# Kernel optimization log

Measured on AMD Instinct MI355X. Metric: run time of the kernel, lower is better.

The kernel has to match this reference:

```python
import jax, jax.numpy as jnp
import numpy as np

N, E, NF, EF, G = 50000, 400000, 128, 64, 200


def _leaky(x):
    return jax.nn.leaky_relu(x, 0.01)


def _edge_softmax(logits, dst, n):
    # softmax over edges grouped by destination node; logits: [E, 1]
    m = jax.ops.segment_max(logits, dst, num_segments=n)
    m = jnp.where(jnp.isfinite(m), m, 0.0)  # guard empty segments
    e = jnp.exp(logits - m[dst])
    s = jax.ops.segment_sum(e, dst, num_segments=n)
    return e / s[dst]


def _gru(x, h, Wx, Wh, bx, bh):
    # torch.nn.GRUCell gate order: (r, z, n)
    gx = x @ Wx + bx
    gh = h @ Wh + bh
    H = h.shape[-1]
    r = jax.nn.sigmoid(gx[:, :H] + gh[:, :H])
    z = jax.nn.sigmoid(gx[:, H:2 * H] + gh[:, H:2 * H])
    nn_ = jnp.tanh(gx[:, 2 * H:] + r * gh[:, 2 * H:])
    return (1.0 - z) * nn_ + z * h


def setup_inputs() -> dict:
    key = jax.random.key(0)
    ks = jax.random.split(key, 20)
    f32 = jnp.float32
    w = lambda k, s: (jax.random.normal(k, s) * 0.05).astype(f32)
    z = lambda s: jnp.zeros(s, f32)
    return {
        "node_feats": jax.random.normal(ks[0], (N, NF), f32),
        "edge_feats": jax.random.normal(ks[1], (E, EF), f32),
        "gc_node_W": w(ks[4], (NF, G)), "gc_node_b": z((G,)),
        "gc_e1_W": w(ks[5], (NF + EF, G)), "gc_e1_b": z((G,)),
        "gc_e2_W": w(ks[6], (2 * G, 1)), "gc_e2_b": z((1,)),
        "gc_et_W": w(ks[7], (G, G)), "gc_et_b": z((G,)),
        "gc_gru_Wx": w(ks[8], (G, 3 * G)), "gc_gru_Wh": w(ks[9], (G, 3 * G)),
        "gc_gru_bx": z((3 * G,)), "gc_gru_bh": z((3 * G,)),
        "l1_e_W": w(ks[10], (2 * G, 1)), "l1_e_b": z((1,)),
        "l1_pn_W": w(ks[11], (G, G)), "l1_pn_b": z((G,)),
        "l1_gru_Wx": w(ks[12], (G, 3 * G)), "l1_gru_Wh": w(ks[13], (G, 3 * G)),
        "l1_gru_bx": z((3 * G,)), "l1_gru_bh": z((3 * G,)),
        "l1_bn_g": jnp.ones((G,), f32), "l1_bn_b": z((G,)),
        "src": jax.random.randint(ks[2], (E,), 0, N, jnp.int32),
        "dst": jax.random.randint(ks[3], (E,), 0, N, jnp.int32),
    }


def reference(node_feats, edge_feats,
              gc_node_W, gc_node_b, gc_e1_W, gc_e1_b, gc_e2_W, gc_e2_b,
              gc_et_W, gc_et_b, gc_gru_Wx, gc_gru_Wh, gc_gru_bx, gc_gru_bh,
              l1_e_W, l1_e_b, l1_pn_W, l1_pn_b, l1_gru_Wx, l1_gru_Wh,
              l1_gru_bx, l1_gru_bh, l1_bn_g, l1_bn_b, src, dst):
    n = node_feats.shape[0]
    # ---- GetContext ----
    hv_new = _leaky(node_feats @ gc_node_W + gc_node_b)                      # [N, G]
    he1 = _leaky(jnp.concatenate([node_feats[src], edge_feats], 1)
                 @ gc_e1_W + gc_e1_b)                                        # [E, G]
    logits = _leaky(jnp.concatenate([hv_new[dst], he1], 1)
                    @ gc_e2_W + gc_e2_b)                                     # [E, 1]
    a = _edge_softmax(logits, dst, n)
    e = a * (he1 @ gc_et_W + gc_et_b)
    c = jax.ops.segment_sum(e, dst, num_segments=n)                          # [N, G]
    h0 = jax.nn.relu(_gru(jax.nn.elu(c), hv_new,
                          gc_gru_Wx, gc_gru_Wh, gc_gru_bx, gc_gru_bh))
    # ---- GNNLayer ----
    logits2 = _leaky(jnp.concatenate([h0[dst], h0[src]], 1) @ l1_e_W + l1_e_b)
    a2 = _edge_softmax(logits2, dst, n) + 1.0
    hvp = h0 @ l1_pn_W + l1_pn_b
    c2 = jax.ops.segment_sum(hvp[src] * a2, dst, num_segments=n)
    h1 = jax.nn.relu(_gru(jax.nn.elu(c2), h0,
                          l1_gru_Wx, l1_gru_Wh, l1_gru_bx, l1_gru_bh))
    # BatchNorm1d (training-mode batch stats, eps=1e-5)
    mu = h1.mean(0)
    var = h1.var(0)
    h1 = l1_bn_g * (h1 - mu) / jnp.sqrt(var + 1e-5) + l1_bn_b
    return h0 + h1
```

## Files before the change

kernel.cpp:

```cpp
#include <hip/hip_runtime.h>
#include <math.h>

#define G 200
#define NF 128
#define EF 64

typedef __attribute__((ext_vector_type(8))) short bf16x8;
typedef __attribute__((ext_vector_type(4))) float f32x4;

__device__ __forceinline__ float leakyf(float x) { return x > 0.f ? x : 0.01f * x; }
__device__ __forceinline__ float eluf(float x)   { return x > 0.f ? x : (expf(x) - 1.f); }
__device__ __forceinline__ float sigm(float x)   { return 1.f / (1.f + expf(-x)); }

__device__ __forceinline__ unsigned short f2bf(float x) {
    union { float f; unsigned int u; } v; v.f = x;
    unsigned int r = v.u + 0x7FFF + ((v.u >> 16) & 1);
    return (unsigned short)(r >> 16);
}
__device__ __forceinline__ float bf2f(unsigned short u) {
    union { unsigned int i; float f; } v; v.i = ((unsigned int)u) << 16;
    return v.f;
}
__device__ __forceinline__ unsigned int pk2(float a, float b) {
    return (unsigned int)f2bf(a) | ((unsigned int)f2bf(b) << 16);
}

__global__ __launch_bounds__(256) void tprep_k(
    const float* __restrict__ W, unsigned short* __restrict__ Wt,
    int Kreal, int kpad, int Nstride, int Nreal)
{
    int total = 208 * kpad;
    for (int i = blockIdx.x * 256 + threadIdx.x; i < total; i += gridDim.x * 256) {
        int n = i / kpad, k = i % kpad;
        Wt[i] = (n < Nreal && k < Kreal) ? f2bf(W[(size_t)k * Nstride + n]) : 0;
    }
}

__global__ __launch_bounds__(256) void wgru3_k(
    const float* __restrict__ Wx, const float* __restrict__ Wh,
    unsigned short* __restrict__ Btrz, unsigned short* __restrict__ Btn)
{
    const int total = 512 * 416;
    for (int i = blockIdx.x * 256 + threadIdx.x; i < total; i += gridDim.x * 256) {
        int n = i / 416, k = i % 416;
        float v = 0.f;
        if (n < 416) {
            int gg = (n >= 208) ? 1 : 0;
            int c = n - gg * 208;
            if (c < 200) {
                if (k < 200)                  v = Wx[(size_t)k * 600 + gg * 200 + c];
                else if (k >= 208 && k < 408) v = Wh[(size_t)(k - 208) * 600 + gg * 200 + c];
            }
        }
        Btrz[i] = f2bf(v);

        float u = 0.f;
        int s = n >> 4, cc = n & 15;
        if (s < 26) {
            int c = (s >> 1) * 16 + cc;
            if (c < 200) {
                if (!(s & 1)) { if (k < 200) u = Wx[(size_t)k * 600 + 400 + c]; }
                else { if (k >= 208 && k < 408) u = Wh[(size_t)(k - 208) * 600 + 400 + c]; }
            }
        }
        Btn[i] = f2bf(u);
    }
}

__global__ __launch_bounds__(256) void gpack_k(
    const float* __restrict__ X, const float* __restrict__ H,
    unsigned short* __restrict__ Apk, int M, int Mpad)
{
    const long total = (long)Mpad * 52;
    for (long i = (long)blockIdx.x * 256 + threadIdx.x; i < total;
         i += (long)gridDim.x * 256) {
        int row = (int)(i / 52), ch = (int)(i % 52);
        uint4 u = make_uint4(0, 0, 0, 0);
        if (row < M) {
            if (ch < 25) {
                const float4* xp = (const float4*)(X + (size_t)row * 200 + ch * 8);
                float4 a = xp[0], b = xp[1];
                u.x = pk2(eluf(a.x), eluf(a.y)); u.y = pk2(eluf(a.z), eluf(a.w));
                u.z = pk2(eluf(b.x), eluf(b.y)); u.w = pk2(eluf(b.z), eluf(b.w));
            } else if (ch >= 26 && ch < 51) {
                const float4* hp = (const float4*)(H + (size_t)row * 200 + (ch - 26) * 8);
                float4 a = hp[0], b = hp[1];
                u.x = pk2(a.x, a.y); u.y = pk2(a.z, a.w);
                u.z = pk2(b.x, b.y); u.w = pk2(b.z, b.w);
            }
        }
        *(uint4*)&Apk[(size_t)row * 416 + ch * 8] = u;
    }
}

template <int EPI>
__global__ __launch_bounds__(256) void tgemm_k(
    const unsigned short* __restrict__ Apk,
    const unsigned short* __restrict__ Bt,
    const float* __restrict__ bx, const float* __restrict__ bh,
    unsigned short* __restrict__ RZ,
    float* __restrict__ OUT, int M)
{
    __shared__ __align__(16) unsigned short As[2][128 * 32];
    __shared__ __align__(16) unsigned short Bs[2][128 * 32];

    const int tid = threadIdx.x;
    const int w = tid >> 6, lane = tid & 63, l15 = lane & 15, lq = lane >> 4;
    const int wr = w >> 1, wc = w & 1;
    const int bm = blockIdx.x * 128, bn = blockIdx.y * 128;
    const int r0 = tid >> 2, sl = tid & 3;

    f32x4 acc[4][4];
#pragma unroll
    for (int a = 0; a < 4; ++a)
#pragma unroll
        for (int b = 0; b < 4; ++b) acc[a][b] = (f32x4){0.f, 0.f, 0.f, 0.f};

    {
        uint4 pa0 = *(const uint4*)&Apk[(size_t)(bm + r0) * 416 + sl * 8];
        uint4 pa1 = *(const uint4*)&Apk[(size_t)(bm + 64 + r0) * 416 + sl * 8];
        uint4 pb0 = *(const uint4*)&Bt[(size_t)(bn + r0) * 416 + sl * 8];
        uint4 pb1 = *(const uint4*)&Bt[(size_t)(bn + 64 + r0) * 416 + sl * 8];
        int w0 = sl ^ ((r0 >> 1) & 3), w1 = sl ^ (((r0 + 64) >> 1) & 3);
        *(uint4*)&As[0][r0 * 32 + w0 * 8] = pa0;
        *(uint4*)&As[0][(r0 + 64) * 32 + w1 * 8] = pa1;
        *(uint4*)&Bs[0][r0 * 32 + w0 * 8] = pb0;
        *(uint4*)&Bs[0][(r0 + 64) * 32 + w1 * 8] = pb1;
    }
    __syncthreads();

    int cur = 0;
    for (int c = 0; c < 13; ++c) {
        uint4 pa0, pa1, pb0, pb1;
        if (c < 12) {
            int kc = (c + 1) * 32;
            pa0 = *(const uint4*)&Apk[(size_t)(bm + r0) * 416 + kc + sl * 8];
            pa1 = *(const uint4*)&Apk[(size_t)(bm + 64 + r0) * 416 + kc + sl * 8];
            pb0 = *(const uint4*)&Bt[(size_t)(bn + r0) * 416 + kc + sl * 8];
            pb1 = *(const uint4*)&Bt[(size_t)(bn + 64 + r0) * 416 + kc + sl * 8];
        }
        bf16x8 af[4], bfr[4];
#pragma unroll
        for (int s = 0; s < 4; ++s) {
            int ra = wr * 64 + s * 16 + l15;
            af[s] = *(const bf16x8*)&As[cur][ra * 32 + (lq ^ ((ra >> 1) & 3)) * 8];
            int rb = wc * 64 + s * 16 + l15;
            bfr[s] = *(const bf16x8*)&Bs[cur][rb * 32 + (lq ^ ((rb >> 1) & 3)) * 8];
        }
#pragma unroll
        for (int sr = 0; sr < 4; ++sr)
#pragma unroll
            for (int sc = 0; sc < 4; ++sc)
                acc[sr][sc] = __builtin_amdgcn_mfma_f32_16x16x32_bf16(
                    af[sr], bfr[sc], acc[sr][sc], 0, 0, 0);

        if (c < 12) {
            int nb = cur ^ 1;
            int w0 = sl ^ ((r0 >> 1) & 3), w1 = sl ^ (((r0 + 64) >> 1) & 3);
            *(uint4*)&As[nb][r0 * 32 + w0 * 8] = pa0;
            *(uint4*)&As[nb][(r0 + 64) * 32 + w1 * 8] = pa1;
            *(uint4*)&Bs[nb][r0 * 32 + w0 * 8] = pb0;
            *(uint4*)&Bs[nb][(r0 + 64) * 32 + w1 * 8] = pb1;
        }
        __syncthreads();
        cur ^= 1;
    }

    if (EPI == 0) {
#pragma unroll
        for (int sr = 0; sr < 4; ++sr)
#pragma unroll
            for (int sc = 0; sc < 4; ++sc) {
                int col = bn + wc * 64 + sc * 16 + l15;
                if (col >= 416) continue;
                float bsum = (col < 208) ? (bx[col] + bh[col])
                                         : (bx[col - 8] + bh[col - 8]);
#pragma unroll
                for (int i = 0; i < 4; ++i) {
                    int row = bm + wr * 64 + sr * 16 + lq * 4 + i;
                    if (row < M)
                        RZ[(size_t)row * 416 + col] = f2bf(sigm(acc[sr][sc][i] + bsum));
                }
            }
    } else {
#pragma unroll
        for (int p = 0; p < 2; ++p) {
            int sglob = (bn >> 4) + wc * 4 + 2 * p;
            int cc = (sglob >> 1) * 16 + l15;
            if (cc >= 200) continue;
            float bxn = bx[400 + cc], bhn = bh[400 + cc];
#pragma unroll
            for (int sr = 0; sr < 4; ++sr)
#pragma unroll
                for (int i = 0; i < 4; ++i) {
                    int row = bm + wr * 64 + sr * 16 + lq * 4 + i;
                    if (row >= M) continue;
                    float rr = bf2f(RZ[(size_t)row * 416 + cc]);
                    float zz = bf2f(RZ[(size_t)row * 416 + 208 + cc]);
                    float hh = bf2f(Apk[(size_t)row * 416 + 208 + cc]);
                    float nn = tanhf(acc[sr][2 * p][i] + bxn +
                                     rr * (acc[sr][2 * p + 1][i] + bhn));
                    float o = (1.f - zz) * nn + zz * hh;
                    OUT[(size_t)row * 200 + cc] = fmaxf(o, 0.f);
                }
        }
    }
}

__global__ __launch_bounds__(256) void hist_k(
    const int* __restrict__ dst, int* __restrict__ cnt, int E)
{
    int i = blockIdx.x * 256 + threadIdx.x;
    if (i < E) atomicAdd(&cnt[dst[i]], 1);
}

__global__ __launch_bounds__(256) void scan_k(
    const int* __restrict__ cnt, int* __restrict__ offs,
    int* __restrict__ cursor, int Nn)
{
    __shared__ int wsum[4];
    const int tid = threadIdx.x;
    const int lane = tid & 63, wv = tid >> 6;
    int carry = 0;
    const int CH = 8;
    for (int base = 0; base < Nn; base += 256 * CH) {
        int v[CH]; int tsum = 0;
        int i0 = base + tid * CH;
#pragma unroll
        for (int j = 0; j < CH; ++j) {
            v[j] = (i0 + j < Nn) ? cnt[i0 + j] : 0;
            tsum += v[j];
        }
        int x = tsum;
        for (int off = 1; off < 64; off <<= 1) {
            int t = __shfl_up(x, off);
            if (lane >= off) x += t;
        }
        if (lane == 63) wsum[wv] = x;
        __syncthreads();
        int wbase = 0;
#pragma unroll
        for (int wq = 0; wq < 4; ++wq) wbase += (wq < wv) ? wsum[wq] : 0;
        int gtot = wsum[0] + wsum[1] + wsum[2] + wsum[3];
        int run = carry + wbase + (x - tsum);
#pragma unroll
        for (int j = 0; j < CH; ++j) {
            int idx = i0 + j;
            if (idx < Nn) { offs[idx] = run; cursor[idx] = run; }
            run += v[j];
        }
        carry += gtot;
        __syncthreads();
    }
    if (tid == 0) offs[Nn] = carry;
}

__global__ __launch_bounds__(256) void scatter_k(
    const int* __restrict__ src, const int* __restrict__ dst,
    int* __restrict__ cursor, int* __restrict__ eidC,
    int* __restrict__ srcC, int* __restrict__ dstC, int E)
{
    int i = blockIdx.x * 256 + threadIdx.x;
    if (i < E) {
        int d = dst[i];
        int pos = atomicAdd(&cursor[d], 1);
        eidC[pos] = i; srcC[pos] = src[i]; dstC[pos] = d;
    }
}

__global__ __launch_bounds__(256) void mgemm_k(
    const float* __restrict__ X, const unsigned short* __restrict__ Wt,
    const float* __restrict__ bias, float* __restrict__ OUT,
    int M, int Kreal, int kch, int astr, int leaky,
    const float* __restrict__ xdiv)
{
    __shared__ __align__(16) unsigned short A[64 * 232];
    const int tid = threadIdx.x;
    const int w = tid >> 6, lane = tid & 63, l15 = lane & 15, lq = lane >> 4;
    const int bm = blockIdx.x * 64;
    const int kpad = kch * 32;
    const int nch8 = Kreal >> 3;

    for (int i = tid; i < 64 * nch8; i += 256) {
        int r = i / nch8, ch = i % nch8;
        int grow = bm + r;
        uint4 u = make_uint4(0, 0, 0, 0);
        if (grow < M) {
            const float4* xp = (const float4*)(X + (size_t)grow * Kreal + ch * 8);
            float inv = 1.f;
            if (xdiv) { float dv = xdiv[grow]; inv = (dv > 0.f) ? 1.f / dv : 0.f; }
            float4 a = xp[0], b = xp[1];
            u.x = pk2(a.x * inv, a.y * inv); u.y = pk2(a.z * inv, a.w * inv);
            u.z = pk2(b.x * inv, b.y * inv); u.w = pk2(b.z * inv, b.w * inv);
        }
        *(uint4*)&A[r * astr + ch * 8] = u;
    }
    if (tid < 64) {
        for (int p = Kreal; p < kpad; p += 8)
            *(uint4*)&A[tid * astr + p] = make_uint4(0, 0, 0, 0);
    }
    __syncthreads();

    const int arow = (w * 16 + l15) * astr;
    f32x4 acc[13];
#pragma unroll
    for (int t = 0; t < 13; ++t) acc[t] = (f32x4){0.f, 0.f, 0.f, 0.f};

    for (int c = 0; c < kch; ++c) {
        bf16x8 a = *(const bf16x8*)&A[arow + c * 32 + lq * 8];
#pragma unroll
        for (int t = 0; t < 13; ++t) {
            bf16x8 b = *(const bf16x8*)&Wt[(size_t)(t * 16 + l15) * kpad + c * 32 + lq * 8];
            acc[t] = __builtin_amdgcn_mfma_f32_16x16x32_bf16(a, b, acc[t], 0, 0, 0);
        }
    }

    float rg[4];
#pragma unroll
    for (int i = 0; i < 4; ++i) {
        int grow = bm + w * 16 + lq * 4 + i;
        rg[i] = 1.f;
        if (xdiv && grow < M) rg[i] = (xdiv[grow] > 0.f) ? 1.f : 0.f;
    }

#pragma unroll
    for (int t = 0; t < 13; ++t) {
        int col = t * 16 + l15;
        if (col >= 200) continue;
        float bs = bias[col];
#pragma unroll
        for (int i = 0; i < 4; ++i) {
            int grow = bm + w * 16 + lq * 4 + i;
            if (grow >= M) continue;
            float v = acc[t][i] + bs * rg[i];
            OUT[(size_t)grow * 200 + col] = leaky ? leakyf(v) : v;
        }
    }
}

__global__ __launch_bounds__(256) void hd_k(
    const float* __restrict__ x, const float* __restrict__ W,
    float* __restrict__ hd, int Nn)
{
    int wid = blockIdx.x * 4 + (threadIdx.x >> 6);
    int lane = threadIdx.x & 63;
    if (wid >= Nn) return;
    float s = 0.f;
    for (int j = lane; j < G; j += 64) s += x[(size_t)wid * G + j] * W[j];
    for (int off = 32; off; off >>= 1) s += __shfl_down(s, off);
    if (lane == 0) hd[wid] = s;
}

__global__ __launch_bounds__(256) void edgefuse2_k(
    const float* __restrict__ node, const float* __restrict__ edgef,
    const int* __restrict__ srcC, const int* __restrict__ dstC,
    const int* __restrict__ eidC,
    const unsigned short* __restrict__ W1t, const float* __restrict__ b1,
    const float* __restrict__ e2W, const float* __restrict__ e2b,
    const float* __restrict__ hd,
    float* __restrict__ sden, float* __restrict__ hacc, int E)
{
    __shared__ __align__(16) unsigned short U[64 * 216];
    __shared__ __align__(16) unsigned short Wt[208 * 40];
    __shared__ float rowlg[64];
    __shared__ float pexp_s[64];
    __shared__ int   dst_s[64];

    const int tid  = threadIdx.x;
    const int w    = tid >> 6;
    const int lane = tid & 63;
    const int l15  = lane & 15;
    const int lq   = lane >> 4;
    const int eb   = blockIdx.x * 64;

    {
        const int r4 = tid >> 2, q = tid & 3;
        const int pos = eb + r4;
        if (pos < E) {
            const int se = srcC[pos];
            const int ei = eidC[pos];
            const float4* np = (const float4*)(node + (size_t)se * NF);
            const float4* ep = (const float4*)(edgef + (size_t)ei * EF);
            uint4* rowp = (uint4*)(U + r4 * 216);
#pragma unroll
            for (int i = 0; i < 4; ++i) {
                float4 a = np[q * 8 + 2 * i];
                float4 b = np[q * 8 + 2 * i + 1];
                uint4 u; u.x = pk2(a.x, a.y); u.y = pk2(a.z, a.w);
                u.z = pk2(b.x, b.y); u.w = pk2(b.z, b.w);
                rowp[q * 4 + i] = u;
            }
            uint4* edp = (uint4*)(U + r4 * 216 + 128);
#pragma unroll
            for (int i = 0; i < 2; ++i) {
                float4 a = ep[q * 4 + 2 * i];
                float4 b = ep[q * 4 + 2 * i + 1];
                uint4 u; u.x = pk2(a.x, a.y); u.y = pk2(a.z, a.w);
                u.z = pk2(b.x, b.y); u.w = pk2(b.z, b.w);
                edp[q * 2 + i] = u;
            }
        } else {
            uint4 z = make_uint4(0, 0, 0, 0);
            uint4* rowp = (uint4*)(U + r4 * 216);
#pragma unroll
            for (int i = 0; i < 4; ++i) rowp[q * 4 + i] = z;
            uint4* edp = (uint4*)(U + r4 * 216 + 128);
            edp[q * 2] = z; edp[q * 2 + 1] = z;
        }
        if (tid < 64) dst_s[tid] = (eb + tid < E) ? dstC[eb + tid] : -1;
    }
    __syncthreads();

    f32x4 acc[13];
#pragma unroll
    for (int t = 0; t < 13; ++t) acc[t] = (f32x4){0.f, 0.f, 0.f, 0.f};

    for (int c = 0; c < 6; ++c) {
        for (int q = tid; q < 832; q += 256) {
            int n = q >> 2, s = q & 3;
            *(uint4*)(Wt + n * 40 + s * 8) =
                *(const uint4*)(W1t + (size_t)n * 192 + c * 32 + s * 8);
        }
        __syncthreads();
        bf16x8 a = *(const bf16x8*)(U + (w * 16 + l15) * 216 + c * 32 + lq * 8);
#pragma unroll
        for (int t = 0; t < 13; ++t) {
            bf16x8 b = *(const bf16x8*)(Wt + (t * 16 + l15) * 40 + lq * 8);
            acc[t] = __builtin_amdgcn_mfma_f32_16x16x32_bf16(a, b, acc[t], 0, 0, 0);
        }
        __syncthreads();
    }

    float p[4] = {0.f, 0.f, 0.f, 0.f};
#pragma unroll
    for (int t = 0; t < 13; ++t) {
        const int col = t * 16 + l15;
#pragma unroll
        for (int r = 0; r < 4; ++r) {
            const int row = w * 16 + lq * 4 + r;
            float v = 0.f;
            if (col < 200) {
                v = leakyf(acc[t][r] + b1[col]);
                p[r] = fmaf(v, e2W[200 + col], p[r]);
            }
            U[row * 216 + col] = f2bf(v);
        }
    }
#pragma unroll
    for (int r = 0; r < 4; ++r) {
        p[r] += __shfl_xor(p[r], 1);
        p[r] += __shfl_xor(p[r], 2);
        p[r] += __shfl_xor(p[r], 4);
        p[r] += __shfl_xor(p[r], 8);
    }
    if (l15 == 0) {
#pragma unroll
        for (int r = 0; r < 4; ++r) rowlg[w * 16 + lq * 4 + r] = p[r];
    }
    __syncthreads();

    if (tid < 64) {
        float pe = 0.f;
        if (eb + tid < E) {
            float l = leakyf(rowlg[tid] + hd[dst_s[tid]] + e2b[0]);
            pe = expf(l);
            atomicAdd(&sden[dst_s[tid]], pe);
        }
        pexp_s[tid] = pe;
    }
    __syncthreads();

    if (tid < 200) {
        const int c = tid;
        float s = 0.f;
        int cur = dst_s[0];
        for (int r = 0; r < 64; ++r) {
            int d = dst_s[r];
            if (d < 0) break;
            if (d != cur) {
                atomicAdd(&hacc[(size_t)cur * 200 + c], s);
                s = 0.f; cur = d;
            }
            s = fmaf(pexp_s[r], bf2f(U[r * 216 + c]), s);
        }
        atomicAdd(&hacc[(size_t)cur * 200 + c], s);
    }
}

__global__ __launch_bounds__(256) void layer2_k(
    const float* __restrict__ h0, const float* __restrict__ hvp,
    const float* __restrict__ hd2,
    const float* __restrict__ W, const float* __restrict__ b,
    const int* __restrict__ offs, const int* __restrict__ srcC,
    float* __restrict__ c2, int Nn)
{
    __shared__ float pes[4][64];
    const int wv = threadIdx.x >> 6;
    const int lane = threadIdx.x & 63;
    const int n = blockIdx.x * 4 + wv;
    if (n >= Nn) return;

    const int base = offs[n], end = offs[n + 1];
    const float hdn = hd2[n] + b[0];

    float ssum = 0.f;
    for (int pos = base; pos < end; ++pos) {
        const float* hr = h0 + (size_t)srcC[pos] * 200;
        float part = hr[lane] * W[200 + lane]
                   + hr[64 + lane] * W[264 + lane]
                   + hr[128 + lane] * W[328 + lane];
        if (lane < 8) part += hr[192 + lane] * W[392 + lane];
        for (int off = 32; off; off >>= 1) part += __shfl_xor(part, off);
        float pe = expf(leakyf(part + hdn));
        ssum += pe;
        int i = pos - base;
        if (i < 64 && lane == 0) pes[wv][i] = pe;
    }
    float inv = (end > base) ? 1.f / ssum : 0.f;

    float a0 = 0.f, a1 = 0.f, a2v = 0.f, a3 = 0.f;
    for (int pos = base; pos < end; ++pos) {
        int i = pos - base;
        float pe;
        if (i < 64) pe = pes[wv][i];
        else {
            const float* hr = h0 + (size_t)srcC[pos] * 200;
            float part = hr[lane] * W[200 + lane]
                       + hr[64 + lane] * W[264 + lane]
                       + hr[128 + lane] * W[328 + lane];
            if (lane < 8) part += hr[192 + lane] * W[392 + lane];
            for (int off = 32; off; off >>= 1) part += __shfl_xor(part, off);
            pe = expf(leakyf(part + hdn));
        }
        float aw = pe * inv + 1.f;
        const float* vr = hvp + (size_t)srcC[pos] * 200;
        a0  += aw * vr[lane];
        a1  += aw * vr[64 + lane];
        a2v += aw * vr[128 + lane];
        if (lane < 8) a3 += aw * vr[192 + lane];
    }
    float* out = c2 + (size_t)n * 200;
    out[lane] = a0; out[64 + lane] = a1; out[128 + lane] = a2v;
    if (lane < 8) out[192 + lane] = a3;
}

__global__ __launch_bounds__(256) void bnstat_k(
    const float* __restrict__ h1, float* __restrict__ stats, long total)
{
    __shared__ float ls[2 * G];
    for (int t = threadIdx.x; t < 2 * G; t += 256) ls[t] = 0.f;
    __syncthreads();
    for (long idx = (long)blockIdx.x * 256 + threadIdx.x; idx < total;
         idx += (long)gridDim.x * 256) {
        float v = h1[idx];
        int c = (int)(idx % G);
        atomicAdd(&ls[c], v);
        atomicAdd(&ls[G + c], v * v);
    }
    __syncthreads();
    for (int t = threadIdx.x; t < 2 * G; t += 256) atomicAdd(&stats[t], ls[t]);
}

__global__ __launch_bounds__(256) void final_k(
    float* __restrict__ out, const float* __restrict__ h1,
    const float* __restrict__ stats,
    const float* __restrict__ g, const float* __restrict__ bb, int Nn)
{
    long total = (long)Nn * G;
    for (long idx = (long)blockIdx.x * 256 + threadIdx.x; idx < total;
         idx += (long)gridDim.x * 256) {
        int c = (int)(idx % G);
        float mu  = stats[c] / Nn;
        float var = stats[G + c] / Nn - mu * mu;
        float xh  = (h1[idx] - mu) * rsqrtf(var + 1e-5f);
        out[idx] = out[idx] + g[c] * xh + bb[c];
    }
}

extern "C" void kernel_launch(void* const* d_in, const int* in_sizes, int n_in,
                              void* d_out, int out_size, void* d_ws, size_t ws_size,
                              hipStream_t stream)
{
    const float* node_feats = (const float*)d_in[0];
    const float* edge_feats = (const float*)d_in[1];
    const float* gc_node_W  = (const float*)d_in[2];
    const float* gc_node_b  = (const float*)d_in[3];
    const float* gc_e1_W    = (const float*)d_in[4];
    const float* gc_e1_b    = (const float*)d_in[5];
    const float* gc_e2_W    = (const float*)d_in[6];
    const float* gc_e2_b    = (const float*)d_in[7];
    const float* gc_et_W    = (const float*)d_in[8];
    const float* gc_et_b    = (const float*)d_in[9];
    const float* gc_gru_Wx  = (const float*)d_in[10];
    const float* gc_gru_Wh  = (const float*)d_in[11];
    const float* gc_gru_bx  = (const float*)d_in[12];
    const float* gc_gru_bh  = (const float*)d_in[13];
    const float* l1_e_W     = (const float*)d_in[14];
    const float* l1_e_b     = (const float*)d_in[15];
    const float* l1_pn_W    = (const float*)d_in[16];
    const float* l1_pn_b    = (const float*)d_in[17];
    const float* l1_gru_Wx  = (const float*)d_in[18];
    const float* l1_gru_Wh  = (const float*)d_in[19];
    const float* l1_gru_bx  = (const float*)d_in[20];
    const float* l1_gru_bh  = (const float*)d_in[21];
    const float* l1_bn_g    = (const float*)d_in[22];
    const float* l1_bn_b    = (const float*)d_in[23];
    const int*   src        = (const int*)d_in[24];
    const int*   dst        = (const int*)d_in[25];

    const int Nn = in_sizes[0] / NF;
    const int E  = in_sizes[24];
    const int Mpad = ((Nn + 127) / 128) * 128;

    float* ws = (float*)d_ws;
    size_t o = 0;
    float* hv    = ws + o; o += (size_t)Nn * G;
    float* cbuf  = ws + o; o += ((size_t)Mpad * 416 + 1) / 2;
    unsigned short* rzbuf = (unsigned short*)cbuf;
    float* sden  = ws + o; o += (size_t)Nn;
    float* hd    = ws + o; o += (size_t)Nn;
    float* stats = ws + o; o += 512;
    unsigned short* W1t_g  = (unsigned short*)(ws + o); o += (208 * 192) / 2;
    unsigned short* etWt_g = (unsigned short*)(ws + o); o += (208 * 224) / 2;
    unsigned short* ncWt_g = (unsigned short*)(ws + o); o += (208 * 128) / 2;
    unsigned short* pnWt_g = (unsigned short*)(ws + o); o += (208 * 224) / 2;
    unsigned short* Btrz1  = (unsigned short*)(ws + o); o += (512 * 416) / 2;
    unsigned short* Btn1   = (unsigned short*)(ws + o); o += (512 * 416) / 2;
    unsigned short* Btrz2  = (unsigned short*)(ws + o); o += (512 * 416) / 2;
    unsigned short* Btn2   = (unsigned short*)(ws + o); o += (512 * 416) / 2;
    int* cnt    = (int*)(ws + o); o += (size_t)Nn;
    int* offs   = (int*)(ws + o); o += (size_t)Nn + 1;
    int* cursor = (int*)(ws + o); o += (size_t)Nn;
    int* eidC   = (int*)(ws + o); o += (size_t)E;
    int* srcC   = (int*)(ws + o); o += (size_t)E;
    int* dstC   = (int*)(ws + o); o += (size_t)E;
    unsigned short* apack = (unsigned short*)(ws + o); o += ((size_t)Mpad * 416 + 1) / 2;

    float* h0  = (float*)d_out;
    float* hvp = hv;
    float* h1  = hv;

    const int gN64 = (Nn + 63) / 64;
    const int gE64 = (E + 63) / 64;
    const int gE256 = (E + 255) / 256;
    const int nWaves = (Nn + 3) / 4;
    const long totNG = (long)Nn * G;
    const dim3 gGEMM((Mpad / 128), 4);

    hipMemsetAsync(cnt, 0, (size_t)Nn * sizeof(int), stream);
    tprep_k<<<128, 256, 0, stream>>>(gc_e1_W,   W1t_g,  192, 192, 200, 200);
    tprep_k<<<128, 256, 0, stream>>>(gc_et_W,   etWt_g, 200, 224, 200, 200);
    tprep_k<<<128, 256, 0, stream>>>(gc_node_W, ncWt_g, 128, 128, 200, 200);
    tprep_k<<<128, 256, 0, stream>>>(l1_pn_W,   pnWt_g, 200, 224, 200, 200);
    wgru3_k<<<256, 256, 0, stream>>>(gc_gru_Wx, gc_gru_Wh, Btrz1, Btn1);
    wgru3_k<<<256, 256, 0, stream>>>(l1_gru_Wx, l1_gru_Wh, Btrz2, Btn2);
    hist_k<<<gE256, 256, 0, stream>>>(dst, cnt, E);
    scan_k<<<1, 256, 0, stream>>>(cnt, offs, cursor, Nn);
    scatter_k<<<gE256, 256, 0, stream>>>(src, dst, cursor, eidC, srcC, dstC, E);

    hipMemsetAsync(sden, 0, (size_t)Nn * sizeof(float), stream);
    hipMemsetAsync(cbuf, 0, (size_t)Nn * G * sizeof(float), stream);
    hipMemsetAsync(stats, 0, 512 * sizeof(float), stream);

    mgemm_k<<<gN64, 256, 0, stream>>>(node_feats, ncWt_g, gc_node_b, hv,
                                      Nn, 128, 4, 136, 1, nullptr);
    hd_k<<<nWaves, 256, 0, stream>>>(hv, gc_e2_W, hd, Nn);

    edgefuse2_k<<<gE64, 256, 0, stream>>>(
        node_feats, edge_feats, srcC, dstC, eidC,
        W1t_g, gc_e1_b, gc_e2_W, gc_e2_b, hd, sden, cbuf, E);

    mgemm_k<<<gN64, 256, 0, stream>>>(cbuf, etWt_g, gc_et_b, cbuf,
                                      Nn, 200, 7, 232, 0, sden);

    gpack_k<<<2048, 256, 0, stream>>>(cbuf, hv, apack, Nn, Mpad);
    tgemm_k<0><<<gGEMM, 256, 0, stream>>>(apack, Btrz1, gc_gru_bx, gc_gru_bh,
                                          rzbuf, nullptr, Nn);
    tgemm_k<1><<<gGEMM, 256, 0, stream>>>(apack, Btn1, gc_gru_bx, gc_gru_bh,
                                          rzbuf, h0, Nn);

    hd_k<<<nWaves, 256, 0, stream>>>(h0, l1_e_W, hd, Nn);

    mgemm_k<<<gN64, 256, 0, stream>>>(h0, pnWt_g, l1_pn_b, hvp,
                                      Nn, 200, 7, 232, 0, nullptr);

    layer2_k<<<nWaves, 256, 0, stream>>>(h0, hvp, hd, l1_e_W, l1_e_b,
                                         offs, srcC, cbuf, Nn);

    gpack_k<<<2048, 256, 0, stream>>>(cbuf, h0, apack, Nn, Mpad);
    tgemm_k<0><<<gGEMM, 256, 0, stream>>>(apack, Btrz2, l1_gru_bx, l1_gru_bh,
                                          rzbuf, nullptr, Nn);
    tgemm_k<1><<<gGEMM, 256, 0, stream>>>(apack, Btn2, l1_gru_bx, l1_gru_bh,
                                          rzbuf, h1, Nn);

    bnstat_k<<<2048, 256, 0, stream>>>(h1, stats, totNG);
    final_k<<<2048, 256, 0, stream>>>((float*)d_out, h1, stats,
                                      l1_bn_g, l1_bn_b, Nn);
}
```

Before: 1.123 ms.

## Precompute per-node source logits, read weights directly, and simplify BN stats

Layer-2 attention logits are split algebraically into a per-destination term and a per-source scalar computed once per node. The edge loops now read one float per edge instead of a 200-wide row of h0 and skip the per-edge wave reductions. The edge-fused GEMM drops its LDS weight staging and barriers and loads B fragments straight from global memory, which relies on cache hits. Batch-norm statistics move from per-element shared-memory atomics to per-column register accumulation across rows.

Result: slower. 1.209 ms (+7.7%).

```diff
diff --git a/kernel.cpp b/kernel.cpp
--- a/kernel.cpp
+++ b/kernel.cpp
@@ -351,7 +351,7 @@
     if (lane == 0) hd[wid] = s;
 }
 
-__global__ __launch_bounds__(256) void edgefuse2_k(
+__global__ __launch_bounds__(256) void edgefuse3_k(
     const float* __restrict__ node, const float* __restrict__ edgef,
     const int* __restrict__ srcC, const int* __restrict__ dstC,
     const int* __restrict__ eidC,
@@ -361,7 +361,6 @@
     float* __restrict__ sden, float* __restrict__ hacc, int E)
 {
     __shared__ __align__(16) unsigned short U[64 * 216];
-    __shared__ __align__(16) unsigned short Wt[208 * 40];
     __shared__ float rowlg[64];
     __shared__ float pexp_s[64];
     __shared__ int   dst_s[64];
@@ -416,19 +415,12 @@
     for (int t = 0; t < 13; ++t) acc[t] = (f32x4){0.f, 0.f, 0.f, 0.f};
 
     for (int c = 0; c < 6; ++c) {
-        for (int q = tid; q < 832; q += 256) {
-            int n = q >> 2, s = q & 3;
-            *(uint4*)(Wt + n * 40 + s * 8) =
-                *(const uint4*)(W1t + (size_t)n * 192 + c * 32 + s * 8);
-        }
-        __syncthreads();
         bf16x8 a = *(const bf16x8*)(U + (w * 16 + l15) * 216 + c * 32 + lq * 8);
 #pragma unroll
         for (int t = 0; t < 13; ++t) {
-            bf16x8 b = *(const bf16x8*)(Wt + (t * 16 + l15) * 40 + lq * 8);
+            bf16x8 b = *(const bf16x8*)&W1t[(size_t)(t * 16 + l15) * 192 + c * 32 + lq * 8];
             acc[t] = __builtin_amdgcn_mfma_f32_16x16x32_bf16(a, b, acc[t], 0, 0, 0);
         }
-        __syncthreads();
     }
 
     float p[4] = {0.f, 0.f, 0.f, 0.f};
@@ -487,14 +479,13 @@
     }
 }
 
-__global__ __launch_bounds__(256) void layer2_k(
-    const float* __restrict__ h0, const float* __restrict__ hvp,
-    const float* __restrict__ hd2,
-    const float* __restrict__ W, const float* __restrict__ b,
+__global__ __launch_bounds__(256) void layer2b_k(
+    const float* __restrict__ hvp,
+    const float* __restrict__ hd2, const float* __restrict__ hs,
+    const float* __restrict__ b,
     const int* __restrict__ offs, const int* __restrict__ srcC,
     float* __restrict__ c2, int Nn)
 {
-    __shared__ float pes[4][64];
     const int wv = threadIdx.x >> 6;
     const int lane = threadIdx.x & 63;
     const int n = blockIdx.x * 4 + wv;
@@ -503,37 +494,18 @@
     const int base = offs[n], end = offs[n + 1];
     const float hdn = hd2[n] + b[0];
 
-    float ssum = 0.f;
-    for (int pos = base; pos < end; ++pos) {
-        const float* hr = h0 + (size_t)srcC[pos] * 200;
-        float part = hr[lane] * W[200 + lane]
-                   + hr[64 + lane] * W[264 + lane]
-                   + hr[128 + lane] * W[328 + lane];
-        if (lane < 8) part += hr[192 + lane] * W[392 + lane];
-        for (int off = 32; off; off >>= 1) part += __shfl_xor(part, off);
-        float pe = expf(leakyf(part + hdn));
-        ssum += pe;
-        int i = pos - base;
-        if (i < 64 && lane == 0) pes[wv][i] = pe;
-    }
-    float inv = (end > base) ? 1.f / ssum : 0.f;
+    float ss = 0.f;
+    for (int pos = base + lane; pos < end; pos += 64)
+        ss += expf(leakyf(hdn + hs[srcC[pos]]));
+    for (int off = 32; off; off >>= 1) ss += __shfl_xor(ss, off);
+    float inv = (end > base) ? 1.f / ss : 0.f;
 
     float a0 = 0.f, a1 = 0.f, a2v = 0.f, a3 = 0.f;
     for (int pos = base; pos < end; ++pos) {
-        int i = pos - base;
-        float pe;
-        if (i < 64) pe = pes[wv][i];
-        else {
-            const float* hr = h0 + (size_t)srcC[pos] * 200;
-            float part = hr[lane] * W[200 + lane]
-                       + hr[64 + lane] * W[264 + lane]
-                       + hr[128 + lane] * W[328 + lane];
-            if (lane < 8) part += hr[192 + lane] * W[392 + lane];
-            for (int off = 32; off; off >>= 1) part += __shfl_xor(part, off);
-            pe = expf(leakyf(part + hdn));
-        }
+        int sidx = srcC[pos];
+        float pe = expf(leakyf(hdn + hs[sidx]));
         float aw = pe * inv + 1.f;
-        const float* vr = hvp + (size_t)srcC[pos] * 200;
+        const float* vr = hvp + (size_t)sidx * 200;
         a0  += aw * vr[lane];
         a1  += aw * vr[64 + lane];
         a2v += aw * vr[128 + lane];
@@ -541,24 +513,21 @@
     }
     float* out = c2 + (size_t)n * 200;
     out[lane] = a0; out[64 + lane] = a1; out[128 + lane] = a2v;
-    if (lane < 8) out[192 + lane] = a3;
-}
-
-__global__ __launch_bounds__(256) void bnstat_k(
-    const float* __restrict__ h1, float* __restrict__ stats, long total)
-{
-    __shared__ float ls[2 * G];
-    for (int t = threadIdx.x; t < 2 * G; t += 256) ls[t] = 0.f;
-    __syncthreads();
-    for (long idx = (long)blockIdx.x * 256 + threadIdx.x; idx < total;
-         idx += (long)gridDim.x * 256) {
-        float v = h1[idx];
-        int c = (int)(idx % G);
-        atomicAdd(&ls[c], v);
-        atomicAdd(&ls[G + c], v * v);
-    }
-    __syncthreads();
-    for (int t = threadIdx.x; t < 2 * G; t += 256) atomicAdd(&stats[t], ls[t]);
+    if (lane < 8) a3 += 0.f, out[192 + lane] = a3;
+}
+
+__global__ __launch_bounds__(256) void bnstat2_k(
+    const float* __restrict__ h1, float* __restrict__ stats, int Nn)
+{
+    const int c = threadIdx.x;
+    if (c >= 200) return;
+    float s = 0.f, s2 = 0.f;
+    for (int r = blockIdx.x; r < Nn; r += gridDim.x) {
+        float v = h1[(size_t)r * 200 + c];
+        s += v; s2 += v * v;
+    }
+    atomicAdd(&stats[c], s);
+    atomicAdd(&stats[G + c], s2);
 }
 
 __global__ __launch_bounds__(256) void final_k(
@@ -619,6 +588,7 @@
     unsigned short* rzbuf = (unsigned short*)cbuf;
     float* sden  = ws + o; o += (size_t)Nn;
     float* hd    = ws + o; o += (size_t)Nn;
+    float* hs    = ws + o; o += (size_t)Nn;
     float* stats = ws + o; o += 512;
     unsigned short* W1t_g  = (unsigned short*)(ws + o); o += (208 * 192) / 2;
     unsigned short* etWt_g = (unsigned short*)(ws + o); o += (208 * 224) / 2;
@@ -666,7 +636,7 @@
                                       Nn, 128, 4, 136, 1, nullptr);
     hd_k<<<nWaves, 256, 0, stream>>>(hv, gc_e2_W, hd, Nn);
 
-    edgefuse2_k<<<gE64, 256, 0, stream>>>(
+    edgefuse3_k<<<gE64, 256, 0, stream>>>(
         node_feats, edge_feats, srcC, dstC, eidC,
         W1t_g, gc_e1_b, gc_e2_W, gc_e2_b, hd, sden, cbuf, E);
 
@@ -680,12 +650,13 @@
                                           rzbuf, h0, Nn);
 
     hd_k<<<nWaves, 256, 0, stream>>>(h0, l1_e_W, hd, Nn);
+    hd_k<<<nWaves, 256, 0, stream>>>(h0, l1_e_W + 200, hs, Nn);
 
     mgemm_k<<<gN64, 256, 0, stream>>>(h0, pnWt_g, l1_pn_b, hvp,
                                       Nn, 200, 7, 232, 0, nullptr);
 
-    layer2_k<<<nWaves, 256, 0, stream>>>(h0, hvp, hd, l1_e_W, l1_e_b,
-                                         offs, srcC, cbuf, Nn);
+    layer2b_k<<<nWaves, 256, 0, stream>>>(hvp, hd, hs, l1_e_b,
+                                          offs, srcC, cbuf, Nn);
 
     gpack_k<<<2048, 256, 0, stream>>>(cbuf, h0, apack, Nn, Mpad);
     tgemm_k<0><<<gGEMM, 256, 0, stream>>>(apack, Btrz2, l1_gru_bx, l1_gru_bh,
@@ -693,7 +664,7 @@
     tgemm_k<1><<<gGEMM, 256, 0, stream>>>(apack, Btn2, l1_gru_bx, l1_gru_bh,
                                           rzbuf, h1, Nn);
 
-    bnstat_k<<<2048, 256, 0, stream>>>(h1, stats, totNG);
+    bnstat2_k<<<512, 256, 0, stream>>>(h1, stats, Nn);
     final_k<<<2048, 256, 0, stream>>>((float*)d_out, h1, stats,
                                       l1_bn_g, l1_bn_b, Nn);
 }
```
